# Kernel optimization log

Hardware: AMD Instinct MI355X
Metric: run time of the kernel (lower is better)

## Reference

```python
import jax, jax.numpy as jnp
import numpy as np

MARGIN = 1.0  # config['margin']


def setup_inputs() -> dict:
    key = jax.random.key(0)
    k1, k2 = jax.random.split(key)
    features = jax.random.normal(k1, (1024, 512), dtype=jnp.float32)
    labels = jax.random.randint(k2, (1024,), 0, 32)
    return {"features": features, "labels": labels}


def _cdist(x):
    # Pairwise euclidean distances, matching torch.cdist; zero-distance
    # entries (e.g., the diagonal) get zero gradient like torch's backward.
    sq = jnp.sum(x * x, axis=-1)
    d2 = sq[:, None] + sq[None, :] - 2.0 * (x @ x.T)
    d2 = jnp.maximum(d2, 0.0)
    safe = jnp.where(d2 > 0.0, d2, 1.0)
    return jnp.where(d2 > 0.0, jnp.sqrt(safe), 0.0)


def reference(features, labels):
    n = features.shape[0]
    dist = _cdist(features)                                   # [N, N]
    pos = (labels[:, None] == labels[None, :]).astype(features.dtype)  # includes diagonal, as in the torch code
    neg = 1.0 - pos

    # loss = sum_i sum_{p in pos(i)} sum_{k in neg(i)} relu(d[i,p] - d[i,k] + margin)
    # Stream over anchors i to avoid materializing the [N, N, N] broadcast.
    def per_anchor(args):
        di, pi, ni = args  # each [N]
        t = jax.nn.relu(di[:, None] - di[None, :] + MARGIN)   # [N_pos_axis, N_neg_axis]
        return jnp.sum(t * (pi[:, None] * ni[None, :]))

    losses = jax.lax.map(per_anchor, (dist, pos, neg))        # [N]
    return jnp.sum(losses) / (n + 1e-8)
```

## Files before the change

### kernel.cpp

```cpp
#include <hip/hip_runtime.h>
#include <math.h>

#define MARGIN 1.0f
#define N_MAX 1024
#define BK 64
#define LSTR 72

typedef short short8 __attribute__((ext_vector_type(8)));
typedef unsigned short ushort8 __attribute__((ext_vector_type(8)));
typedef float floatx16 __attribute__((ext_vector_type(16)));

__device__ inline unsigned short bf16_rne(float x) {
  unsigned u = __float_as_uint(x);
  unsigned r = (u + 0x7FFF + ((u >> 16) & 1)) >> 16;
  return (unsigned short)r;
}
__device__ inline float bf16_to_f32(unsigned short h) {
  return __uint_as_float(((unsigned)h) << 16);
}

__global__ __launch_bounds__(64) void conv_kernel(
    const float* __restrict__ f, unsigned short* __restrict__ fhi,
    unsigned short* __restrict__ flo, float* __restrict__ sq, int D) {
  int row = blockIdx.x;
  int lane = threadIdx.x;
  const float* fr = f + (size_t)row * D;
  unsigned short* hr = fhi + (size_t)row * D;
  unsigned short* lr = flo + (size_t)row * D;

  float acc = 0.f;
  for (int c0 = lane * 4; c0 < D; c0 += 64 * 4) {
    float4 v = *(const float4*)(fr + c0);
    float xs[4] = {v.x, v.y, v.z, v.w};
    unsigned short hs[4], ls[4];
#pragma unroll
    for (int e = 0; e < 4; ++e) {
      float x = xs[e];
      acc += x * x;
      unsigned short h = bf16_rne(x);
      hs[e] = h;
      ls[e] = bf16_rne(x - bf16_to_f32(h));
    }
    *(ushort4*)(hr + c0) = make_ushort4(hs[0], hs[1], hs[2], hs[3]);
    *(ushort4*)(lr + c0) = make_ushort4(ls[0], ls[1], ls[2], ls[3]);
  }
  for (int off = 32; off > 0; off >>= 1) acc += __shfl_down(acc, off, 64);
  if (lane == 0) sq[row] = acc;
}

__global__ __launch_bounds__(256) void dist_kernel(
    const unsigned short* __restrict__ fhi, const unsigned short* __restrict__ flo,
    const float* __restrict__ sqv, float* __restrict__ dist, int N, int D) {
  __shared__ unsigned short Ah[64][LSTR];
  __shared__ unsigned short Al[64][LSTR];
  __shared__ unsigned short Bh[64][LSTR];
  __shared__ unsigned short Bl[64][LSTR];

  const int tid = threadIdx.x;
  const int rowBase = blockIdx.y * 64;
  const int colBase = blockIdx.x * 64;

  const int sr = tid & 63;
  const int sc = (tid >> 6) * 16;

  const int w = tid >> 6;
  const int lane = tid & 63;
  const int wr = (w >> 1) * 32;
  const int wc = (w & 1) * 32;
  const int arow = wr + (lane & 31);
  const int brow = wc + (lane & 31);
  const int kgrp = (lane >> 5) * 8;

  floatx16 acc = {};

  for (int k0 = 0; k0 < D; k0 += BK) {
    const size_t ga = (size_t)(rowBase + sr) * D + k0 + sc;
    const size_t gb = (size_t)(colBase + sr) * D + k0 + sc;
    ushort8 ah0 = *(const ushort8*)(fhi + ga);
    ushort8 ah1 = *(const ushort8*)(fhi + ga + 8);
    ushort8 al0 = *(const ushort8*)(flo + ga);
    ushort8 al1 = *(const ushort8*)(flo + ga + 8);
    ushort8 bh0 = *(const ushort8*)(fhi + gb);
    ushort8 bh1 = *(const ushort8*)(fhi + gb + 8);
    ushort8 bl0 = *(const ushort8*)(flo + gb);
    ushort8 bl1 = *(const ushort8*)(flo + gb + 8);
    __syncthreads();
    *(ushort8*)&Ah[sr][sc] = ah0; *(ushort8*)&Ah[sr][sc + 8] = ah1;
    *(ushort8*)&Al[sr][sc] = al0; *(ushort8*)&Al[sr][sc + 8] = al1;
    *(ushort8*)&Bh[sr][sc] = bh0; *(ushort8*)&Bh[sr][sc + 8] = bh1;
    *(ushort8*)&Bl[sr][sc] = bl0; *(ushort8*)&Bl[sr][sc + 8] = bl1;
    __syncthreads();

#pragma unroll
    for (int kk = 0; kk < BK / 16; ++kk) {
      const int ko = kk * 16 + kgrp;
      short8 ahf = *(const short8*)&Ah[arow][ko];
      short8 alf = *(const short8*)&Al[arow][ko];
      short8 bhf = *(const short8*)&Bh[brow][ko];
      short8 blf = *(const short8*)&Bl[brow][ko];
      acc = __builtin_amdgcn_mfma_f32_32x32x16_bf16(ahf, bhf, acc, 0, 0, 0);
      acc = __builtin_amdgcn_mfma_f32_32x32x16_bf16(ahf, blf, acc, 0, 0, 0);
      acc = __builtin_amdgcn_mfma_f32_32x32x16_bf16(alf, bhf, acc, 0, 0, 0);
    }
  }

  const int col = colBase + wc + (lane & 31);
  const float sqc = sqv[col];
#pragma unroll
  for (int r = 0; r < 16; ++r) {
    const int row = rowBase + wr + (r & 3) + 8 * (r >> 2) + 4 * (lane >> 5);
    float d2 = sqv[row] + sqc - 2.0f * acc[r];
    d2 = d2 > 0.f ? d2 : 0.f;
    dist[(size_t)row * N + col] = sqrtf(d2);
  }
}

__global__ __launch_bounds__(256) void anchor_loss_kernel(
    const float* __restrict__ dist, const int* __restrict__ labels,
    float* __restrict__ partial, int N) {
  const int i = blockIdx.x;
  const int tid = threadIdx.x;
  const int lane = tid & 63;

  __shared__ float dpos[N_MAX];
  __shared__ float dneg[N_MAX];
  __shared__ int cnt[2];
  __shared__ float red[4];

  if (tid < 2) cnt[tid] = 0;
  __syncthreads();

  const int lab = labels[i];
  const float* drow = dist + (size_t)i * N;

  for (int jb = 0; jb < N; jb += 256) {
    int j = jb + tid;
    bool valid = j < N;
    float d = valid ? drow[j] : 0.f;
    bool isPos = valid && (labels[j & (N_MAX - 1)] == lab);
    bool isNeg = valid && !isPos;

    unsigned long long mp = __ballot(isPos);
    unsigned long long mn = __ballot(isNeg);
    unsigned long long lt = (1ull << lane) - 1ull;

    int base_p = 0, base_n = 0;
    if (lane == 0) {
      base_p = atomicAdd(&cnt[0], __popcll(mp));
      base_n = atomicAdd(&cnt[1], __popcll(mn));
    }
    base_p = __shfl(base_p, 0, 64);
    base_n = __shfl(base_n, 0, 64);

    if (isPos) dpos[base_p + __popcll(mp & lt)] = d + MARGIN;
    if (isNeg) dneg[base_n + __popcll(mn & lt)] = d;
  }
  __syncthreads();

  const int np = cnt[0], nn = cnt[1];

  float dk[4];
#pragma unroll
  for (int e = 0; e < 4; ++e) {
    int k = tid + 256 * e;
    dk[e] = (k < nn) ? dneg[k] : 1e30f;
  }

  float accv = 0.f;
  for (int p = 0; p < np; ++p) {
    float t = dpos[p];
#pragma unroll
    for (int e = 0; e < 4; ++e) {
      float v = t - dk[e];
      accv += (v > 0.f) ? v : 0.f;
    }
  }

  for (int off = 32; off > 0; off >>= 1) accv += __shfl_down(accv, off, 64);
  if (lane == 0) red[tid >> 6] = accv;
  __syncthreads();
  if (tid == 0) partial[i] = red[0] + red[1] + red[2] + red[3];
}

__global__ __launch_bounds__(256) void final_reduce_kernel(
    const float* __restrict__ partial, float* __restrict__ out, int N) {
  float acc = 0.f;
  for (int j = threadIdx.x; j < N; j += 256) acc += partial[j];
  for (int off = 32; off > 0; off >>= 1) acc += __shfl_down(acc, off, 64);
  __shared__ float red[4];
  if ((threadIdx.x & 63) == 0) red[threadIdx.x >> 6] = acc;
  __syncthreads();
  if (threadIdx.x == 0) {
    double s = (double)red[0] + (double)red[1] + (double)red[2] + (double)red[3];
    out[0] = (float)(s / ((double)N + 1e-8));
  }
}

extern "C" void kernel_launch(void* const* d_in, const int* in_sizes, int n_in,
                              void* d_out, int out_size, void* d_ws, size_t ws_size,
                              hipStream_t stream) {
  const float* f = (const float*)d_in[0];
  const int* labels = (const int*)d_in[1];
  int N = in_sizes[1];
  int D = in_sizes[0] / N;
  float* out = (float*)d_out;

  unsigned short* fhi = (unsigned short*)d_ws;
  unsigned short* flo = fhi + (size_t)N * D;
  float* sq = (float*)(flo + (size_t)N * D);
  float* dist = sq + N;
  float* partial = dist + (size_t)N * N;

  conv_kernel<<<N, 64, 0, stream>>>(f, fhi, flo, sq, D);
  dim3 grid(N / 64, N / 64);
  dist_kernel<<<grid, 256, 0, stream>>>(fhi, flo, sq, dist, N, D);
  anchor_loss_kernel<<<N, 256, 0, stream>>>(dist, labels, partial, N);
  final_reduce_kernel<<<1, 256, 0, stream>>>(partial, out, N);
}
```

Baseline: 85.14 us.

## Use k-chunk-major bf16 layout and double-buffered LDS prefetch in distance GEMM

```diff
diff --git a/kernel.cpp b/kernel.cpp
--- a/kernel.cpp
+++ b/kernel.cpp
@@ -4,7 +4,6 @@
 #define MARGIN 1.0f
 #define N_MAX 1024
 #define BK 64
-#define LSTR 72
 
 typedef short short8 __attribute__((ext_vector_type(8)));
 typedef unsigned short ushort8 __attribute__((ext_vector_type(8)));
@@ -21,94 +20,100 @@
 
 __global__ __launch_bounds__(64) void conv_kernel(
     const float* __restrict__ f, unsigned short* __restrict__ fhi,
-    unsigned short* __restrict__ flo, float* __restrict__ sq, int D) {
-  int row = blockIdx.x;
-  int lane = threadIdx.x;
-  const float* fr = f + (size_t)row * D;
-  unsigned short* hr = fhi + (size_t)row * D;
-  unsigned short* lr = flo + (size_t)row * D;
-
+    unsigned short* __restrict__ flo, float* __restrict__ sq, int N, int D) {
+  const int r = blockIdx.x;
+  const int t = threadIdx.x;
   float acc = 0.f;
-  for (int c0 = lane * 4; c0 < D; c0 += 64 * 4) {
-    float4 v = *(const float4*)(fr + c0);
-    float xs[4] = {v.x, v.y, v.z, v.w};
-    unsigned short hs[4], ls[4];
-#pragma unroll
-    for (int e = 0; e < 4; ++e) {
+  if (t * 8 < D) {
+    const float* src = f + (size_t)r * D + t * 8;
+    float4 v0 = *(const float4*)(src);
+    float4 v1 = *(const float4*)(src + 4);
+    float xs[8] = {v0.x, v0.y, v0.z, v0.w, v1.x, v1.y, v1.z, v1.w};
+    ushort8 hs, ls;
+#pragma unroll
+    for (int e = 0; e < 8; ++e) {
       float x = xs[e];
       acc += x * x;
       unsigned short h = bf16_rne(x);
       hs[e] = h;
       ls[e] = bf16_rne(x - bf16_to_f32(h));
     }
-    *(ushort4*)(hr + c0) = make_ushort4(hs[0], hs[1], hs[2], hs[3]);
-    *(ushort4*)(lr + c0) = make_ushort4(ls[0], ls[1], ls[2], ls[3]);
+    const size_t off = ((size_t)t * N + r) * 8;
+    *(ushort8*)(fhi + off) = hs;
+    *(ushort8*)(flo + off) = ls;
   }
   for (int off = 32; off > 0; off >>= 1) acc += __shfl_down(acc, off, 64);
-  if (lane == 0) sq[row] = acc;
+  if (t == 0) sq[r] = acc;
 }
 
 __global__ __launch_bounds__(256) void dist_kernel(
     const unsigned short* __restrict__ fhi, const unsigned short* __restrict__ flo,
     const float* __restrict__ sqv, float* __restrict__ dist, int N, int D) {
-  __shared__ unsigned short Ah[64][LSTR];
-  __shared__ unsigned short Al[64][LSTR];
-  __shared__ unsigned short Bh[64][LSTR];
-  __shared__ unsigned short Bl[64][LSTR];
+  __shared__ ushort8 T[2][4][8][64];
 
   const int tid = threadIdx.x;
+  const int w = tid >> 6;
+  const int lane = tid & 63;
   const int rowBase = blockIdx.y * 64;
   const int colBase = blockIdx.x * 64;
 
-  const int sr = tid & 63;
-  const int sc = (tid >> 6) * 16;
-
-  const int w = tid >> 6;
-  const int lane = tid & 63;
+  const unsigned short* srcs[4] = {fhi, flo, fhi, flo};
+  const int bases[4] = {rowBase, rowBase, colBase, colBase};
+
   const int wr = (w >> 1) * 32;
   const int wc = (w & 1) * 32;
-  const int arow = wr + (lane & 31);
-  const int brow = wc + (lane & 31);
-  const int kgrp = (lane >> 5) * 8;
+  const int m = lane & 31;
+  const int h = lane >> 5;
+
+  ushort8 regs[8];
+
+  auto loadRegs = [&](int k0) {
+    const int c0 = k0 >> 3;
+#pragma unroll
+    for (int s = 0; s < 8; ++s) {
+      const int a = s >> 1;
+      const int c = (w << 1) | (s & 1);
+      regs[s] = *(const ushort8*)(srcs[a] + ((size_t)(c0 + c) * N + bases[a] + lane) * 8);
+    }
+  };
+  auto storeRegs = [&](int b) {
+#pragma unroll
+    for (int s = 0; s < 8; ++s) {
+      const int a = s >> 1;
+      const int c = (w << 1) | (s & 1);
+      T[b][a][c][lane] = regs[s];
+    }
+  };
 
   floatx16 acc = {};
+  int b = 0;
+
+  loadRegs(0);
+  storeRegs(0);
 
   for (int k0 = 0; k0 < D; k0 += BK) {
-    const size_t ga = (size_t)(rowBase + sr) * D + k0 + sc;
-    const size_t gb = (size_t)(colBase + sr) * D + k0 + sc;
-    ushort8 ah0 = *(const ushort8*)(fhi + ga);
-    ushort8 ah1 = *(const ushort8*)(fhi + ga + 8);
-    ushort8 al0 = *(const ushort8*)(flo + ga);
-    ushort8 al1 = *(const ushort8*)(flo + ga + 8);
-    ushort8 bh0 = *(const ushort8*)(fhi + gb);
-    ushort8 bh1 = *(const ushort8*)(fhi + gb + 8);
-    ushort8 bl0 = *(const ushort8*)(flo + gb);
-    ushort8 bl1 = *(const ushort8*)(flo + gb + 8);
+    if (k0 + BK < D) loadRegs(k0 + BK);
     __syncthreads();
-    *(ushort8*)&Ah[sr][sc] = ah0; *(ushort8*)&Ah[sr][sc + 8] = ah1;
-    *(ushort8*)&Al[sr][sc] = al0; *(ushort8*)&Al[sr][sc + 8] = al1;
-    *(ushort8*)&Bh[sr][sc] = bh0; *(ushort8*)&Bh[sr][sc + 8] = bh1;
-    *(ushort8*)&Bl[sr][sc] = bl0; *(ushort8*)&Bl[sr][sc + 8] = bl1;
-    __syncthreads();
-
 #pragma unroll
     for (int kk = 0; kk < BK / 16; ++kk) {
-      const int ko = kk * 16 + kgrp;
-      short8 ahf = *(const short8*)&Ah[arow][ko];
-      short8 alf = *(const short8*)&Al[arow][ko];
-      short8 bhf = *(const short8*)&Bh[brow][ko];
-      short8 blf = *(const short8*)&Bl[brow][ko];
+      const int c = 2 * kk + h;
+      short8 ahf = *(const short8*)&T[b][0][c][wr + m];
+      short8 alf = *(const short8*)&T[b][1][c][wr + m];
+      short8 bhf = *(const short8*)&T[b][2][c][wc + m];
+      short8 blf = *(const short8*)&T[b][3][c][wc + m];
       acc = __builtin_amdgcn_mfma_f32_32x32x16_bf16(ahf, bhf, acc, 0, 0, 0);
       acc = __builtin_amdgcn_mfma_f32_32x32x16_bf16(ahf, blf, acc, 0, 0, 0);
       acc = __builtin_amdgcn_mfma_f32_32x32x16_bf16(alf, bhf, acc, 0, 0, 0);
     }
-  }
-
-  const int col = colBase + wc + (lane & 31);
+    if (k0 + BK < D) storeRegs(b ^ 1);
+    b ^= 1;
+  }
+
+  const int col = colBase + wc + m;
   const float sqc = sqv[col];
 #pragma unroll
   for (int r = 0; r < 16; ++r) {
-    const int row = rowBase + wr + (r & 3) + 8 * (r >> 2) + 4 * (lane >> 5);
+    const int row = rowBase + wr + (r & 3) + 8 * (r >> 2) + 4 * h;
     float d2 = sqv[row] + sqc - 2.0f * acc[r];
     d2 = d2 > 0.f ? d2 : 0.f;
     dist[(size_t)row * N + col] = sqrtf(d2);
@@ -211,7 +216,7 @@
   float* dist = sq + N;
   float* partial = dist + (size_t)N * N;
 
-  conv_kernel<<<N, 64, 0, stream>>>(f, fhi, flo, sq, D);
+  conv_kernel<<<N, 64, 0, stream>>>(f, fhi, flo, sq, N, D);
   dim3 grid(N / 64, N / 64);
   dist_kernel<<<grid, 256, 0, stream>>>(fhi, flo, sq, dist, N, D);
   anchor_loss_kernel<<<N, 256, 0, stream>>>(dist, labels, partial, N);
```

New measurement: 78.67 us. -7.6%, faster.
